# Performance work log

Measured on AMD Instinct MI355X. Metric: run time of the kernel, lower is better.

## Reference

```python
import jax, jax.numpy as jnp
import numpy as np

D_MODEL = 1024
N_HEAD = 16
DH = D_MODEL // N_HEAD


def setup_inputs() -> dict:
    key = jax.random.key(0)
    ks = jax.random.split(key, 5)
    B, T = 4, 2048
    scale = 0.02
    return {
        "x": jax.random.normal(ks[0], (B, T, D_MODEL), dtype=jnp.float32),
        "Wqkv": jax.random.normal(ks[1], (D_MODEL, 3 * D_MODEL), dtype=jnp.float32) * scale,
        "bqkv": jnp.zeros((3 * D_MODEL,), dtype=jnp.float32),
        "Wout": jax.random.normal(ks[2], (D_MODEL, D_MODEL), dtype=jnp.float32) * scale,
        "bout": jnp.zeros((D_MODEL,), dtype=jnp.float32),
    }


def reference(x, Wqkv, bqkv, Wout, bout):
    B, T, C = x.shape
    qkv = x @ Wqkv + bqkv  # [B,T,3C]
    q, k, v = jnp.split(qkv, 3, axis=2)
    # [B,T,C] -> [B,H,T,dh]
    def heads(t):
        return t.reshape(B, T, N_HEAD, DH).transpose(0, 2, 1, 3)
    q, k, v = heads(q), heads(k), heads(v)
    scores = jnp.einsum("bhqd,bhkd->bhqk", q, k) / jnp.sqrt(jnp.float32(DH))
    causal = jnp.tril(jnp.ones((T, T), dtype=bool))  # [T,T]
    neg = jnp.finfo(scores.dtype).min
    scores = jnp.where(causal[None, None, :, :], scores, neg)
    A = jax.nn.softmax(scores, axis=-1)
    y = jnp.einsum("bhqk,bhkd->bhqd", A, v)
    y = y.transpose(0, 2, 1, 3).reshape(B, T, C)
    return y @ Wout + bout
```

## Files before the change

### kernel.cpp

```cpp
#include <hip/hip_runtime.h>
#include <hip/hip_bf16.h>

typedef float f32x4 __attribute__((ext_vector_type(4)));
typedef float f32x16 __attribute__((ext_vector_type(16)));
typedef short s16x8 __attribute__((ext_vector_type(8)));
typedef short s16x4 __attribute__((ext_vector_type(4)));
typedef unsigned int u32x4 __attribute__((ext_vector_type(4)));

#define B_ 4
#define T_ 2048
#define C_ 1024
#define H_ 16
#define DH_ 64
#define M_ (B_*T_)
#define N3_ (3*C_)

static __device__ __forceinline__ short f2bf(float f) {
    __hip_bfloat16 h = __float2bfloat16(f);
    return *reinterpret_cast<short*>(&h);
}

static __device__ __forceinline__ unsigned pack2(float lo, float hi) {
    unsigned r;
    asm("v_cvt_pk_bf16_f32 %0, %1, %2" : "=v"(r) : "v"(lo), "v"(hi));
    return r;
}

static __device__ __forceinline__ void gload16(const void* g, void* l) {
    __builtin_amdgcn_global_load_lds(
        (const __attribute__((address_space(1))) void*)g,
        (__attribute__((address_space(3))) void*)l, 16, 0, 0);
}

static __device__ __forceinline__ s16x8 lds_frag(const short* base, int row, int chunk) {
    return *(const s16x8*)&base[(row << 6) + ((chunk ^ (row & 7)) << 3)];
}


__global__ __launch_bounds__(256) void cast_f32_bf16(
    const float* __restrict__ in, short* __restrict__ out, int n8)
{
    int i = blockIdx.x * 256 + threadIdx.x;
    if (i >= n8) return;
    float4 a = *(const float4*)&in[i * 8];
    float4 b = *(const float4*)&in[i * 8 + 4];
    s16x8 o = { f2bf(a.x), f2bf(a.y), f2bf(a.z), f2bf(a.w),
                f2bf(b.x), f2bf(b.y), f2bf(b.z), f2bf(b.w) };
    *(s16x8*)&out[i * 8] = o;
}

__global__ __launch_bounds__(256) void transpose_cast(
    const float* __restrict__ src, short* __restrict__ dst, int K, int N)
{
    __shared__ short t[64][66];
    int tid = threadIdx.x;
    int n0 = blockIdx.x * 64, k0 = blockIdx.y * 64;
    #pragma unroll
    for (int p = 0; p < 4; ++p) {
        int cid = tid + p * 256;
        int r = cid >> 4, c4 = cid & 15;
        float4 v = *(const float4*)&src[(size_t)(k0 + r) * N + n0 + c4 * 4];
        t[r][c4 * 4 + 0] = f2bf(v.x);
        t[r][c4 * 4 + 1] = f2bf(v.y);
        t[r][c4 * 4 + 2] = f2bf(v.z);
        t[r][c4 * 4 + 3] = f2bf(v.w);
    }
    __syncthreads();
    #pragma unroll
    for (int p = 0; p < 4; ++p) {
        int cid = tid + p * 256;
        int r = cid >> 4, c4 = cid & 15;
        s16x4 ov;
        #pragma unroll
        for (int j = 0; j < 4; ++j) ov[j] = t[c4 * 4 + j][r];
        *(s16x4*)&dst[(size_t)(n0 + r) * K + k0 + c4 * 4] = ov;
    }
}


template<int MODE>
__global__ __launch_bounds__(256) void gemm_bt(
    const short* __restrict__ A, const short* __restrict__ Bt,
    const float* __restrict__ bias, float* __restrict__ out,
    short* __restrict__ qout, short* __restrict__ kout, short* __restrict__ vout)
{
    const int K = 1024;
    __shared__ short As[128 * 64];
    __shared__ short Bs[128 * 64];
    int tid = threadIdx.x;
    int lane = tid & 63, w = tid >> 6;
    int d = lane & 15, g = lane >> 4;
    int wm = w >> 1, wn = w & 1;

    int gx = gridDim.x;
    int lid = blockIdx.y * gx + blockIdx.x;
    int chunk = (gx * gridDim.y) >> 3;
    int sl = (lid & 7) * chunk + (lid >> 3);
    int m0 = (sl / gx) * 128, n0 = (sl % gx) * 128;

    f32x4 acc[4][4];
    #pragma unroll
    for (int i = 0; i < 4; ++i)
        #pragma unroll
        for (int j = 0; j < 4; ++j) acc[i][j] = (f32x4){0.f, 0.f, 0.f, 0.f};

    for (int kt = 0; kt < K; kt += 64) {
        #pragma unroll
        for (int p = 0; p < 4; ++p) {
            int cid = p * 256 + tid;
            int r = cid >> 3, c8 = cid & 7;
            int co = (c8 ^ (r & 7)) << 3;
            int dofs = (p * 256 + (tid & ~63)) * 8;
            gload16(&A[(size_t)(m0 + r) * K + kt + co], &As[dofs]);
            gload16(&Bt[(size_t)(n0 + r) * K + kt + co], &Bs[dofs]);
        }
        __syncthreads();
        #pragma unroll
        for (int ks = 0; ks < 2; ++ks) {
            s16x8 af[4], bf[4];
            #pragma unroll
            for (int i = 0; i < 4; ++i) {
                af[i] = lds_frag(As, wm * 64 + i * 16 + d, ks * 4 + g);
                bf[i] = lds_frag(Bs, wn * 64 + i * 16 + d, ks * 4 + g);
            }
            #pragma unroll
            for (int mi = 0; mi < 4; ++mi)
                #pragma unroll
                for (int ni = 0; ni < 4; ++ni)
                    acc[mi][ni] = __builtin_amdgcn_mfma_f32_16x16x32_bf16(
                        af[mi], bf[ni], acc[mi][ni], 0, 0, 0);
        }
        __syncthreads();
    }

    #pragma unroll
    for (int mi = 0; mi < 4; ++mi)
        #pragma unroll
        for (int ni = 0; ni < 4; ++ni) {
            int gn = n0 + wn * 64 + ni * 16 + d;
            float bv = bias[gn];
            int gm0 = m0 + wm * 64 + mi * 16 + g * 4;
            if (MODE == 0) {
                #pragma unroll
                for (int r = 0; r < 4; ++r)
                    out[(size_t)(gm0 + r) * 1024 + gn] = acc[mi][ni][r] + bv;
            } else {
                int which = gn >> 10, cc = gn & 1023;
                int h = cc >> 6, dh = cc & 63;
                int b = gm0 >> 11;
                if (which == 2) {
                    int g2 = ((g & 1) << 1) | (g >> 1);
                    int t0v = (gm0 & 2047) - g * 4 + g2 * 4;
                    s16x4 pv;
                    #pragma unroll
                    for (int r = 0; r < 4; ++r) pv[r] = f2bf(acc[mi][ni][r] + bv);
                    *(s16x4*)&vout[((size_t)(b * 16 + h) * 64 + dh) * 2048 + t0v] = pv;
                } else if (which == 1) {
                    int t0 = gm0 & 2047;
                    #pragma unroll
                    for (int r = 0; r < 4; ++r)
                        kout[((size_t)(b * 16 + h) * 2048 + (t0 + r)) * 64 + dh] =
                            f2bf(acc[mi][ni][r] + bv);
                } else {
                    int t0 = gm0 & 2047;
                    const float SC2 = 0.125f * 1.44269504089f;
                    #pragma unroll
                    for (int r = 0; r < 4; ++r)
                        qout[((size_t)(b * 16 + h) * 2048 + (t0 + r)) * 64 + dh] =
                            f2bf((acc[mi][ni][r] + bv) * SC2);
                }
            }
        }
}


__global__ __launch_bounds__(256, 4) void attn_fwd(
    const short* __restrict__ q, const short* __restrict__ kk,
    const short* __restrict__ vt, short* __restrict__ y)
{
    __shared__ short Ks[2][64 * 64];
    __shared__ short Vs[2][64 * 64];
    int tid = threadIdx.x, w = tid >> 6;
    int lane = tid & 63;
    int q5 = lane & 31, h5 = lane >> 5;
    int bid = blockIdx.x;
    int idx = bid >> 3;
    int qt = 15 - (idx >> 3);
    int bh = ((idx & 7) << 3) | (bid & 7);
    int b = bh >> 4, hh = bh & 15;
    const size_t hb = (size_t)bh * 2048 * 64;
    int nt = 2 * qt + 2;
    int qrow = qt * 128 + w * 32;
    int qg = qrow + q5;

    s16x8 qf[4];
    #pragma unroll
    for (int s = 0; s < 4; ++s)
        qf[s] = *(const s16x8*)&q[hb + (size_t)qg * 64 + 16 * s + 8 * h5];

    f32x16 oA, oB;
    #pragma unroll
    for (int i = 0; i < 16; ++i) { oA[i] = 0.f; oB[i] = 0.f; }
    float l = 0.f;

    #define STAGE(buf, kt2) do { \
        _Pragma("unroll") \
        for (int p = 0; p < 2; ++p) { \
            int cid = p * 256 + tid; \
            int r__ = cid >> 3, c8__ = cid & 7; \
            int co__ = (c8__ ^ (r__ & 7)) << 3; \
            int dofs__ = (p * 256 + (tid & ~63)) * 8; \
            gload16(&kk[hb + (size_t)((kt2) * 64 + r__) * 64 + co__], &Ks[buf][dofs__]); \
            gload16(&vt[hb + (size_t)r__ * 2048 + (kt2) * 64 + co__], &Vs[buf][dofs__]); \
        } \
    } while (0)

    STAGE(0, 0);
    int cur = 0;

    #pragma unroll 1
    for (int t = 0; t < nt; ++t) {
        if (t + 1 < nt) {
            STAGE(cur ^ 1, t + 1);
            asm volatile("s_waitcnt vmcnt(4)" ::: "memory");
        } else {
            asm volatile("s_waitcnt vmcnt(0)" ::: "memory");
        }
        __builtin_amdgcn_s_barrier();

        if (t * 64 <= qrow + 31) {
            const short* Kb = Ks[cur];
            const short* Vb = Vs[cur];

            f32x16 sA, sB;
            #pragma unroll
            for (int i = 0; i < 16; ++i) { sA[i] = 0.f; sB[i] = 0.f; }
            #pragma unroll
            for (int s = 0; s < 4; ++s) {
                sA = __builtin_amdgcn_mfma_f32_32x32x16_bf16(
                    lds_frag(Kb, q5, 2 * s + h5), qf[s], sA, 0, 0, 0);
                sB = __builtin_amdgcn_mfma_f32_32x32x16_bf16(
                    lds_frag(Kb, 32 + q5, 2 * s + h5), qf[s], sB, 0, 0, 0);
            }

            float eA[16], eB[16];
            float S = 0.f;
            if (t * 64 + 63 > qrow) {
                #pragma unroll
                for (int rg = 0; rg < 16; ++rg) {
                    int kg = t * 64 + (rg & 3) + 8 * (rg >> 2) + 4 * h5;
                    float a = exp2f(sA[rg]); if (kg > qg) a = 0.f;
                    float c = exp2f(sB[rg]); if (kg + 32 > qg) c = 0.f;
                    eA[rg] = a; eB[rg] = c; S += a + c;
                }
            } else {
                #pragma unroll
                for (int rg = 0; rg < 16; ++rg) {
                    float a = exp2f(sA[rg]);
                    float c = exp2f(sB[rg]);
                    eA[rg] = a; eB[rg] = c; S += a + c;
                }
            }
            l += S;

            unsigned wdA[8], wdB[8];
            #pragma unroll
            for (int m = 0; m < 4; ++m) {
                wdA[2 * m]     = pack2(eA[4 * m],     eA[4 * m + 1]);
                wdA[2 * m + 1] = pack2(eA[4 * m + 2], eA[4 * m + 3]);
                wdB[2 * m]     = pack2(eB[4 * m],     eB[4 * m + 1]);
                wdB[2 * m + 1] = pack2(eB[4 * m + 2], eB[4 * m + 3]);
            }

            #pragma unroll
            for (int kc = 0; kc < 4; ++kc) {
                const unsigned* wsrc = (kc < 2) ? wdA : wdB;
                int o4 = (kc & 1) << 2;
                u32x4 pw = {wsrc[o4], wsrc[o4 + 1], wsrc[o4 + 2], wsrc[o4 + 3]};
                s16x8 pb = __builtin_bit_cast(s16x8, pw);
                oA = __builtin_amdgcn_mfma_f32_32x32x16_bf16(
                    lds_frag(Vb, q5, 2 * kc + h5), pb, oA, 0, 0, 0);
                oB = __builtin_amdgcn_mfma_f32_32x32x16_bf16(
                    lds_frag(Vb, 32 + q5, 2 * kc + h5), pb, oB, 0, 0, 0);
            }
        }

        __builtin_amdgcn_s_barrier();
        cur ^= 1;
    }

    l += __shfl_xor(l, 32);
    float rl = 1.0f / l;

    short* yp = &y[(size_t)(b * 2048 + qg) * 1024 + hh * 64];
    #pragma unroll
    for (int m = 0; m < 4; ++m) {
        s16x4 v0, v1;
        #pragma unroll
        for (int i = 0; i < 4; ++i) {
            v0[i] = f2bf(oA[4 * m + i] * rl);
            v1[i] = f2bf(oB[4 * m + i] * rl);
        }
        *(s16x4*)&yp[8 * m + 4 * h5] = v0;
        *(s16x4*)&yp[32 + 8 * m + 4 * h5] = v1;
    }
    #undef STAGE
}


extern "C" void kernel_launch(void* const* d_in, const int* in_sizes, int n_in,
                              void* d_out, int out_size, void* d_ws, size_t ws_size,
                              hipStream_t stream)
{
    const float* x    = (const float*)d_in[0];
    const float* Wqkv = (const float*)d_in[1];
    const float* bqkv = (const float*)d_in[2];
    const float* Wout = (const float*)d_in[3];
    const float* bout = (const float*)d_in[4];
    float* out = (float*)d_out;

    char* ws = (char*)d_ws;
    short* xbf   = (short*)ws;  ws += (size_t)M_ * C_ * 2;
    short* wqkvT = (short*)ws;  ws += (size_t)N3_ * C_ * 2;
    short* woutT = (short*)ws;  ws += (size_t)C_ * C_ * 2;
    short* qb    = (short*)ws;  ws += (size_t)M_ * C_ * 2;
    short* kb    = (short*)ws;  ws += (size_t)M_ * C_ * 2;
    short* vtb   = (short*)ws;  ws += (size_t)M_ * C_ * 2;
    short* yb    = (short*)ws;  ws += (size_t)M_ * C_ * 2;

    cast_f32_bf16<<<(M_ * C_ / 8 + 255) / 256, 256, 0, stream>>>(x, xbf, M_ * C_ / 8);
    transpose_cast<<<dim3(N3_ / 64, C_ / 64), 256, 0, stream>>>(Wqkv, wqkvT, C_, N3_);
    transpose_cast<<<dim3(C_ / 64, C_ / 64), 256, 0, stream>>>(Wout, woutT, C_, C_);

    gemm_bt<1><<<dim3(N3_ / 128, M_ / 128), 256, 0, stream>>>(
        xbf, wqkvT, bqkv, nullptr, qb, kb, vtb);

    attn_fwd<<<dim3((T_ / 128) * B_ * H_), 256, 0, stream>>>(qb, kb, vtb, yb);

    gemm_bt<0><<<dim3(C_ / 128, M_ / 128), 256, 0, stream>>>(
        yb, woutT, bout, out, nullptr, nullptr, nullptr);
}
```

Measured before the change: 182.5 us.

## Pair long and short causal query tiles per block and refine LDS swizzle

Each attention block now processes two query tiles, a long one (15-pi) and a short one (pi), so every block does the same amount of causal work. This halves the grid to 512 blocks and is meant to remove tail imbalance across CUs. The LDS XOR swizzle gains an extra bit from row bit 3 to reduce bank conflicts, and s_setprio is raised around the MFMA sections to favour matrix issue. In exchange there are fewer blocks available for latency hiding, and the two passes run serially within each block.

```diff
diff --git a/kernel.cpp b/kernel.cpp
--- a/kernel.cpp
+++ b/kernel.cpp
@@ -34,6 +34,13 @@
 
 static __device__ __forceinline__ s16x8 lds_frag(const short* base, int row, int chunk) {
     return *(const s16x8*)&base[(row << 6) + ((chunk ^ (row & 7)) << 3)];
+}
+
+static __device__ __forceinline__ int aswz(int row) {
+    return (row & 7) ^ (((row >> 3) & 1) << 2);
+}
+static __device__ __forceinline__ s16x8 attn_frag(const short* base, int row, int chunk) {
+    return *(const s16x8*)&base[(row << 6) + ((chunk ^ aswz(row)) << 3)];
 }
 
 
@@ -184,125 +191,133 @@
     int lane = tid & 63;
     int q5 = lane & 31, h5 = lane >> 5;
     int bid = blockIdx.x;
-    int idx = bid >> 3;
-    int qt = 15 - (idx >> 3);
-    int bh = ((idx & 7) << 3) | (bid & 7);
+    int pi = (bid >> 3) & 7;
+    int bh = ((bid >> 6) << 3) | (bid & 7);
     int b = bh >> 4, hh = bh & 15;
     const size_t hb = (size_t)bh * 2048 * 64;
-    int nt = 2 * qt + 2;
-    int qrow = qt * 128 + w * 32;
-    int qg = qrow + q5;
-
-    s16x8 qf[4];
-    #pragma unroll
-    for (int s = 0; s < 4; ++s)
-        qf[s] = *(const s16x8*)&q[hb + (size_t)qg * 64 + 16 * s + 8 * h5];
-
-    f32x16 oA, oB;
-    #pragma unroll
-    for (int i = 0; i < 16; ++i) { oA[i] = 0.f; oB[i] = 0.f; }
-    float l = 0.f;
 
     #define STAGE(buf, kt2) do { \
         _Pragma("unroll") \
         for (int p = 0; p < 2; ++p) { \
             int cid = p * 256 + tid; \
             int r__ = cid >> 3, c8__ = cid & 7; \
-            int co__ = (c8__ ^ (r__ & 7)) << 3; \
+            int co__ = (c8__ ^ aswz(r__)) << 3; \
             int dofs__ = (p * 256 + (tid & ~63)) * 8; \
             gload16(&kk[hb + (size_t)((kt2) * 64 + r__) * 64 + co__], &Ks[buf][dofs__]); \
             gload16(&vt[hb + (size_t)r__ * 2048 + (kt2) * 64 + co__], &Vs[buf][dofs__]); \
         } \
     } while (0)
 
-    STAGE(0, 0);
-    int cur = 0;
-
     #pragma unroll 1
-    for (int t = 0; t < nt; ++t) {
-        if (t + 1 < nt) {
-            STAGE(cur ^ 1, t + 1);
-            asm volatile("s_waitcnt vmcnt(4)" ::: "memory");
-        } else {
-            asm volatile("s_waitcnt vmcnt(0)" ::: "memory");
-        }
-        __builtin_amdgcn_s_barrier();
-
-        if (t * 64 <= qrow + 31) {
-            const short* Kb = Ks[cur];
-            const short* Vb = Vs[cur];
-
-            f32x16 sA, sB;
+    for (int pass = 0; pass < 2; ++pass) {
+        int qt = pass ? pi : (15 - pi);
+        int nt = 2 * qt + 2;
+        int qrow = qt * 128 + w * 32;
+        int qg = qrow + q5;
+
+        s16x8 qf[4];
+        #pragma unroll
+        for (int s = 0; s < 4; ++s)
+            qf[s] = *(const s16x8*)&q[hb + (size_t)qg * 64 + 16 * s + 8 * h5];
+
+        f32x16 oA, oB;
+        #pragma unroll
+        for (int i = 0; i < 16; ++i) { oA[i] = 0.f; oB[i] = 0.f; }
+        float l = 0.f;
+
+        STAGE(0, 0);
+        int cur = 0;
+
+        #pragma unroll 1
+        for (int t = 0; t < nt; ++t) {
+            if (t + 1 < nt) {
+                STAGE(cur ^ 1, t + 1);
+                asm volatile("s_waitcnt vmcnt(4)" ::: "memory");
+            } else {
+                asm volatile("s_waitcnt vmcnt(0)" ::: "memory");
+            }
+            __builtin_amdgcn_s_barrier();
+
+            if (t * 64 <= qrow + 31) {
+                const short* Kb = Ks[cur];
+                const short* Vb = Vs[cur];
+
+                f32x16 sA, sB;
+                #pragma unroll
+                for (int i = 0; i < 16; ++i) { sA[i] = 0.f; sB[i] = 0.f; }
+                __builtin_amdgcn_s_setprio(1);
+                #pragma unroll
+                for (int s = 0; s < 4; ++s) {
+                    sA = __builtin_amdgcn_mfma_f32_32x32x16_bf16(
+                        attn_frag(Kb, q5, 2 * s + h5), qf[s], sA, 0, 0, 0);
+                    sB = __builtin_amdgcn_mfma_f32_32x32x16_bf16(
+                        attn_frag(Kb, 32 + q5, 2 * s + h5), qf[s], sB, 0, 0, 0);
+                }
+                __builtin_amdgcn_s_setprio(0);
+
+                float eA[16], eB[16];
+                float S = 0.f;
+                if (t * 64 + 63 > qrow) {
+                    #pragma unroll
+                    for (int rg = 0; rg < 16; ++rg) {
+                        int kg = t * 64 + (rg & 3) + 8 * (rg >> 2) + 4 * h5;
+                        float a = exp2f(sA[rg]); if (kg > qg) a = 0.f;
+                        float c = exp2f(sB[rg]); if (kg + 32 > qg) c = 0.f;
+                        eA[rg] = a; eB[rg] = c; S += a + c;
+                    }
+                } else {
+                    #pragma unroll
+                    for (int rg = 0; rg < 16; ++rg) {
+                        float a = exp2f(sA[rg]);
+                        float c = exp2f(sB[rg]);
+                        eA[rg] = a; eB[rg] = c; S += a + c;
+                    }
+                }
+                l += S;
+
+                unsigned wdA[8], wdB[8];
+                #pragma unroll
+                for (int m = 0; m < 4; ++m) {
+                    wdA[2 * m]     = pack2(eA[4 * m],     eA[4 * m + 1]);
+                    wdA[2 * m + 1] = pack2(eA[4 * m + 2], eA[4 * m + 3]);
+                    wdB[2 * m]     = pack2(eB[4 * m],     eB[4 * m + 1]);
+                    wdB[2 * m + 1] = pack2(eB[4 * m + 2], eB[4 * m + 3]);
+                }
+
+                __builtin_amdgcn_s_setprio(1);
+                #pragma unroll
+                for (int kc = 0; kc < 4; ++kc) {
+                    const unsigned* wsrc = (kc < 2) ? wdA : wdB;
+                    int o4 = (kc & 1) << 2;
+                    u32x4 pw = {wsrc[o4], wsrc[o4 + 1], wsrc[o4 + 2], wsrc[o4 + 3]};
+                    s16x8 pb = __builtin_bit_cast(s16x8, pw);
+                    oA = __builtin_amdgcn_mfma_f32_32x32x16_bf16(
+                        attn_frag(Vb, q5, 2 * kc + h5), pb, oA, 0, 0, 0);
+                    oB = __builtin_amdgcn_mfma_f32_32x32x16_bf16(
+                        attn_frag(Vb, 32 + q5, 2 * kc + h5), pb, oB, 0, 0, 0);
+                }
+                __builtin_amdgcn_s_setprio(0);
+            }
+
+            __builtin_amdgcn_s_barrier();
+            cur ^= 1;
+        }
+
+        l += __shfl_xor(l, 32);
+        float rl = 1.0f / l;
+
+        short* yp = &y[(size_t)(b * 2048 + qg) * 1024 + hh * 64];
+        #pragma unroll
+        for (int m = 0; m < 4; ++m) {
+            s16x4 v0, v1;
             #pragma unroll
-            for (int i = 0; i < 16; ++i) { sA[i] = 0.f; sB[i] = 0.f; }
-            #pragma unroll
-            for (int s = 0; s < 4; ++s) {
-                sA = __builtin_amdgcn_mfma_f32_32x32x16_bf16(
-                    lds_frag(Kb, q5, 2 * s + h5), qf[s], sA, 0, 0, 0);
-                sB = __builtin_amdgcn_mfma_f32_32x32x16_bf16(
-                    lds_frag(Kb, 32 + q5, 2 * s + h5), qf[s], sB, 0, 0, 0);
-            }
-
-            float eA[16], eB[16];
-            float S = 0.f;
-            if (t * 64 + 63 > qrow) {
-                #pragma unroll
-                for (int rg = 0; rg < 16; ++rg) {
-                    int kg = t * 64 + (rg & 3) + 8 * (rg >> 2) + 4 * h5;
-                    float a = exp2f(sA[rg]); if (kg > qg) a = 0.f;
-                    float c = exp2f(sB[rg]); if (kg + 32 > qg) c = 0.f;
-                    eA[rg] = a; eB[rg] = c; S += a + c;
-                }
-            } else {
-                #pragma unroll
-                for (int rg = 0; rg < 16; ++rg) {
-                    float a = exp2f(sA[rg]);
-                    float c = exp2f(sB[rg]);
-                    eA[rg] = a; eB[rg] = c; S += a + c;
-                }
-            }
-            l += S;
-
-            unsigned wdA[8], wdB[8];
-            #pragma unroll
-            for (int m = 0; m < 4; ++m) {
-                wdA[2 * m]     = pack2(eA[4 * m],     eA[4 * m + 1]);
-                wdA[2 * m + 1] = pack2(eA[4 * m + 2], eA[4 * m + 3]);
-                wdB[2 * m]     = pack2(eB[4 * m],     eB[4 * m + 1]);
-                wdB[2 * m + 1] = pack2(eB[4 * m + 2], eB[4 * m + 3]);
-            }
-
-            #pragma unroll
-            for (int kc = 0; kc < 4; ++kc) {
-                const unsigned* wsrc = (kc < 2) ? wdA : wdB;
-                int o4 = (kc & 1) << 2;
-                u32x4 pw = {wsrc[o4], wsrc[o4 + 1], wsrc[o4 + 2], wsrc[o4 + 3]};
-                s16x8 pb = __builtin_bit_cast(s16x8, pw);
-                oA = __builtin_amdgcn_mfma_f32_32x32x16_bf16(
-                    lds_frag(Vb, q5, 2 * kc + h5), pb, oA, 0, 0, 0);
-                oB = __builtin_amdgcn_mfma_f32_32x32x16_bf16(
-                    lds_frag(Vb, 32 + q5, 2 * kc + h5), pb, oB, 0, 0, 0);
-            }
-        }
-
-        __builtin_amdgcn_s_barrier();
-        cur ^= 1;
-    }
-
-    l += __shfl_xor(l, 32);
-    float rl = 1.0f / l;
-
-    short* yp = &y[(size_t)(b * 2048 + qg) * 1024 + hh * 64];
-    #pragma unroll
-    for (int m = 0; m < 4; ++m) {
-        s16x4 v0, v1;
-        #pragma unroll
-        for (int i = 0; i < 4; ++i) {
-            v0[i] = f2bf(oA[4 * m + i] * rl);
-            v1[i] = f2bf(oB[4 * m + i] * rl);
-        }
-        *(s16x4*)&yp[8 * m + 4 * h5] = v0;
-        *(s16x4*)&yp[32 + 8 * m + 4 * h5] = v1;
+            for (int i = 0; i < 4; ++i) {
+                v0[i] = f2bf(oA[4 * m + i] * rl);
+                v1[i] = f2bf(oB[4 * m + i] * rl);
+            }
+            *(s16x4*)&yp[8 * m + 4 * h5] = v0;
+            *(s16x4*)&yp[32 + 8 * m + 4 * h5] = v1;
+        }
     }
     #undef STAGE
 }
@@ -335,7 +350,7 @@
     gemm_bt<1><<<dim3(N3_ / 128, M_ / 128), 256, 0, stream>>>(
         xbf, wqkvT, bqkv, nullptr, qb, kb, vtb);
 
-    attn_fwd<<<dim3((T_ / 128) * B_ * H_), 256, 0, stream>>>(qb, kb, vtb, yb);
+    attn_fwd<<<dim3(512), 256, 0, stream>>>(qb, kb, vtb, yb);
 
     gemm_bt<0><<<dim3(C_ / 128, M_ / 128), 256, 0, stream>>>(
         yb, woutT, bout, out, nullptr, nullptr, nullptr);
```

Measured after the change: 208.3 us. 1.14x slower.

## Enlarge attention blocks to 256 query rows with 4-stage K/V prefetch pipeline

Applied to the files above, without the earlier changes.

The attention kernel now uses 512-thread blocks covering 256 query rows each, so every K/V tile loaded into shared memory is reused by 8 waves instead of 4. The K/V prefetch ring grows from a double buffer to four stages, issued three tiles ahead. Query tiles are assigned to blocks in a paired order, so block counts per wave balance causal work. MFMA sections are wrapped in s_setprio to favour the matrix work, at the cost of more LDS per block (64KB) and fewer, larger blocks (512), which may reduce occupancy and raise tail imbalance.

```diff
diff --git a/kernel.cpp b/kernel.cpp
--- a/kernel.cpp
+++ b/kernel.cpp
@@ -174,24 +174,33 @@
 }
 
 
-__global__ __launch_bounds__(256, 4) void attn_fwd(
+__global__ __launch_bounds__(512, 4) void attn_fwd(
     const short* __restrict__ q, const short* __restrict__ kk,
     const short* __restrict__ vt, short* __restrict__ y)
 {
-    __shared__ short Ks[2][64 * 64];
-    __shared__ short Vs[2][64 * 64];
+    __shared__ short Ks[4][64 * 64];
+    __shared__ short Vs[4][64 * 64];
     int tid = threadIdx.x, w = tid >> 6;
     int lane = tid & 63;
     int q5 = lane & 31, h5 = lane >> 5;
     int bid = blockIdx.x;
-    int idx = bid >> 3;
-    int qt = 15 - (idx >> 3);
-    int bh = ((idx & 7) << 3) | (bid & 7);
-    int b = bh >> 4, hh = bh & 15;
-    const size_t hb = (size_t)bh * 2048 * 64;
-    int nt = 2 * qt + 2;
-    int qrow = qt * 128 + w * 32;
+    int j = bid >> 6;
+    int qt = (j < 4) ? j : (11 - j);
+    int head = bid & 63;
+    int b = head >> 4, hh = head & 15;
+    const size_t hb = (size_t)head * 2048 * 64;
+    int nt = 4 * qt + 4;
+    int qrow = qt * 256 + w * 32;
     int qg = qrow + q5;
+
+    int r_ = tid >> 3, c8_ = tid & 7;
+    int co_ = (c8_ ^ (r_ & 7)) << 3;
+    int dofs_ = (tid & ~63) * 8;
+
+    #define STAGE(buf, kt2) do { \
+        gload16(&kk[hb + (size_t)((kt2) * 64 + r_) * 64 + co_], &Ks[buf][dofs_]); \
+        gload16(&vt[hb + (size_t)r_ * 2048 + (kt2) * 64 + co_], &Vs[buf][dofs_]); \
+    } while (0)
 
     s16x8 qf[4];
     #pragma unroll
@@ -203,38 +212,26 @@
     for (int i = 0; i < 16; ++i) { oA[i] = 0.f; oB[i] = 0.f; }
     float l = 0.f;
 
-    #define STAGE(buf, kt2) do { \
-        _Pragma("unroll") \
-        for (int p = 0; p < 2; ++p) { \
-            int cid = p * 256 + tid; \
-            int r__ = cid >> 3, c8__ = cid & 7; \
-            int co__ = (c8__ ^ (r__ & 7)) << 3; \
-            int dofs__ = (p * 256 + (tid & ~63)) * 8; \
-            gload16(&kk[hb + (size_t)((kt2) * 64 + r__) * 64 + co__], &Ks[buf][dofs__]); \
-            gload16(&vt[hb + (size_t)r__ * 2048 + (kt2) * 64 + co__], &Vs[buf][dofs__]); \
-        } \
-    } while (0)
-
     STAGE(0, 0);
-    int cur = 0;
+    STAGE(1, 1);
+    STAGE(2, 2);
 
     #pragma unroll 1
     for (int t = 0; t < nt; ++t) {
-        if (t + 1 < nt) {
-            STAGE(cur ^ 1, t + 1);
-            asm volatile("s_waitcnt vmcnt(4)" ::: "memory");
-        } else {
-            asm volatile("s_waitcnt vmcnt(0)" ::: "memory");
-        }
+        int nxt = t + 3;
+        if (nxt >= nt) nxt = nt - 1;
+        STAGE((t + 3) & 3, nxt);
+        asm volatile("s_waitcnt vmcnt(6)" ::: "memory");
         __builtin_amdgcn_s_barrier();
 
         if (t * 64 <= qrow + 31) {
-            const short* Kb = Ks[cur];
-            const short* Vb = Vs[cur];
+            const short* Kb = Ks[t & 3];
+            const short* Vb = Vs[t & 3];
 
             f32x16 sA, sB;
             #pragma unroll
             for (int i = 0; i < 16; ++i) { sA[i] = 0.f; sB[i] = 0.f; }
+            __builtin_amdgcn_s_setprio(1);
             #pragma unroll
             for (int s = 0; s < 4; ++s) {
                 sA = __builtin_amdgcn_mfma_f32_32x32x16_bf16(
@@ -242,6 +239,7 @@
                 sB = __builtin_amdgcn_mfma_f32_32x32x16_bf16(
                     lds_frag(Kb, 32 + q5, 2 * s + h5), qf[s], sB, 0, 0, 0);
             }
+            __builtin_amdgcn_s_setprio(0);
 
             float eA[16], eB[16];
             float S = 0.f;
@@ -272,6 +270,7 @@
                 wdB[2 * m + 1] = pack2(eB[4 * m + 2], eB[4 * m + 3]);
             }
 
+            __builtin_amdgcn_s_setprio(1);
             #pragma unroll
             for (int kc = 0; kc < 4; ++kc) {
                 const unsigned* wsrc = (kc < 2) ? wdA : wdB;
@@ -283,10 +282,10 @@
                 oB = __builtin_amdgcn_mfma_f32_32x32x16_bf16(
                     lds_frag(Vb, 32 + q5, 2 * kc + h5), pb, oB, 0, 0, 0);
             }
+            __builtin_amdgcn_s_setprio(0);
         }
 
         __builtin_amdgcn_s_barrier();
-        cur ^= 1;
     }
 
     l += __shfl_xor(l, 32);
@@ -335,7 +334,7 @@
     gemm_bt<1><<<dim3(N3_ / 128, M_ / 128), 256, 0, stream>>>(
         xbf, wqkvT, bqkv, nullptr, qb, kb, vtb);
 
-    attn_fwd<<<dim3((T_ / 128) * B_ * H_), 256, 0, stream>>>(qb, kb, vtb, yb);
+    attn_fwd<<<dim3(512), 512, 0, stream>>>(qb, kb, vtb, yb);
 
     gemm_bt<0><<<dim3(C_ / 128, M_ / 128), 256, 0, stream>>>(
         yb, woutT, bout, out, nullptr, nullptr, nullptr);
```

After: 188.6 us. 1.03x slower.
